# Kernel tuning notes

Hardware: AMD Instinct MI355X
Metric: run time of the kernel (lower is better)

## Reference

```python
import jax, jax.numpy as jnp
import numpy as np

H = 8
BLEN = 256
NEG = -1e9

def _mask2d(blen, h=32, win=6):
    # precomputed 2D-local mask for tail blocks: query pos in [blen, 2blen),
    # key pos in [0, 2blen); causal + Chebyshev-ish window on a width-h image grid
    cp = np.arange(blen, 2 * blen)[:, None]
    op = np.arange(2 * blen)[None, :]
    causal = op <= cp
    ch, cw = cp // h, cp % h
    oh, ow = op // h, op % h
    ok = causal & (np.abs(ch - oh) <= win) & (np.abs(cw - ow) <= win)
    return np.where(ok, 0.0, NEG).astype(np.float32)

def _causal_mask(blen):
    return np.where(np.tril(np.ones((blen, blen), bool)), 0.0, NEG).astype(np.float32)

def _attn(X, Wq, Wk, Wv, Wo):
    B, L, D = X.shape
    dh = D // H
    split = lambda Y: Y.reshape(B, L, H, dh).transpose(0, 2, 1, 3)  # [B,H,L,dh]
    q = split(X @ Wq) * (dh ** -0.5)
    k = split(X @ Wk)
    v = split(X @ Wv)
    pad = (-L) % BLEN
    if pad:
        q, k, v = (jnp.pad(t, ((0, 0), (0, 0), (0, pad), (0, 0))) for t in (q, k, v))
    Lp = L + pad
    n = Lp // BLEN
    bias1 = jnp.asarray(_causal_mask(BLEN))
    logits1 = jnp.einsum('bhqd,bhkd->bhqk', q[:, :, :BLEN], k[:, :, :BLEN]) + bias1
    first = jax.nn.softmax(logits1, axis=-1) @ v[:, :, :BLEN]  # [B,H,BLEN,dh]
    if n > 1:
        qb = q.reshape(B, H, n, BLEN, dh)
        kb = k.reshape(B, H, n, BLEN, dh)
        vb = v.reshape(B, H, n, BLEN, dh)
        local_k = jnp.concatenate([kb[:, :, :-1], kb[:, :, 1:]], axis=3)  # [B,H,n-1,2B,dh]
        local_v = jnp.concatenate([vb[:, :, :-1], vb[:, :, 1:]], axis=3)
        bias2 = jnp.asarray(_mask2d(BLEN))
        logits2 = jnp.einsum('bhnqd,bhnkd->bhnqk', qb[:, :, 1:], local_k) + bias2
        tail = jnp.einsum('bhnqk,bhnkd->bhnqd', jax.nn.softmax(logits2, axis=-1), local_v)
        tail = tail.reshape(B, H, (n - 1) * BLEN, dh)
        res = jnp.concatenate([first, tail], axis=2)[:, :, :L]
    else:
        res = first[:, :, :L]
    res = res.transpose(0, 2, 1, 3).reshape(B, L, D)
    return res @ Wo

def _ln(x, g, b, eps=1e-6):
    m = x.mean(-1, keepdims=True)
    v = ((x - m) ** 2).mean(-1, keepdims=True)
    return (x - m) / jnp.sqrt(v + eps) * g + b

def setup_inputs() -> dict:
    key = jax.random.key(0)
    ks = jax.random.split(key, 8)
    D, F = 256, 512
    s = 0.02
    return {
        'X': jax.random.normal(ks[0], (32, 1024, D), jnp.float32),
        'Wq': jax.random.normal(ks[1], (D, D), jnp.float32) * s,
        'Wk': jax.random.normal(ks[2], (D, D), jnp.float32) * s,
        'Wv': jax.random.normal(ks[3], (D, D), jnp.float32) * s,
        'Wo': jax.random.normal(ks[4], (D, D), jnp.float32) * s,
        'ln1_g': jnp.ones((D,), jnp.float32),
        'ln1_b': jnp.zeros((D,), jnp.float32),
        'W1': jax.random.normal(ks[5], (D, F), jnp.float32) * s,
        'b1': jnp.zeros((F,), jnp.float32),
        'W2': jax.random.normal(ks[6], (F, D), jnp.float32) * s,
        'b2': jnp.zeros((D,), jnp.float32),
        'ln2_g': jnp.ones((D,), jnp.float32),
        'ln2_b': jnp.zeros((D,), jnp.float32),
    }

def reference(X, Wq, Wk, Wv, Wo, ln1_g, ln1_b, W1, b1, W2, b2, ln2_g, ln2_b):
    y = _attn(X, Wq, Wk, Wv, Wo)
    X = _ln(y + X, ln1_g, ln1_b)
    y = jax.nn.relu(X @ W1 + b1) @ W2 + b2
    return _ln(y + X, ln2_g, ln2_b)
```

## Files before the change

kernel.cpp:

```cpp
#include <hip/hip_runtime.h>

typedef unsigned short u16;
typedef __attribute__((ext_vector_type(8))) short bh8;
typedef __attribute__((ext_vector_type(4))) short s4;
typedef __attribute__((ext_vector_type(4))) short bh4;
typedef __attribute__((ext_vector_type(4))) float fx4;

__device__ __forceinline__ u16 f2b(float f) {
  union { float f; unsigned u; } v; v.f = f;
  unsigned r = v.u + 0x7fffu + ((v.u >> 16) & 1u);
  return (u16)(r >> 16);
}
__device__ __forceinline__ float b2f(u16 h) {
  union { unsigned u; float f; } v; v.u = ((unsigned)h) << 16; return v.f;
}

__device__ __forceinline__ float ex2(float x) {
#if __has_builtin(__builtin_amdgcn_exp2f)
  return __builtin_amdgcn_exp2f(x);
#else
  return __expf(x * 0.6931471805599453f);
#endif
}

__device__ __forceinline__ unsigned cvtpk(float lo, float hi) {
  unsigned r;
  asm("v_cvt_pk_bf16_f32 %0, %1, %2" : "=v"(r) : "v"(lo), "v"(hi));
  return r;
}

#if __has_builtin(__builtin_amdgcn_mfma_f32_16x16x16bf16_1k)
__device__ __forceinline__ fx4 pv_mfma(s4 a, s4 b, fx4 c) {
  return __builtin_amdgcn_mfma_f32_16x16x16bf16_1k(a, b, c, 0, 0, 0);
}
#else
__device__ __forceinline__ fx4 pv_mfma(s4 a, s4 b, fx4 c) {
  asm("v_mfma_f32_16x16x16_bf16 %0, %1, %2, %0" : "+v"(c) : "v"(a), "v"(b));
  return c;
}
#endif

__global__ __launch_bounds__(256) void conv_x_k(const float* __restrict__ X, u16* __restrict__ Xb) {
  int i = blockIdx.x * 256 + threadIdx.x;
  float4 v = ((const float4*)X)[i];
  bh4 o; o[0]=(short)f2b(v.x); o[1]=(short)f2b(v.y); o[2]=(short)f2b(v.z); o[3]=(short)f2b(v.w);
  ((bh4*)Xb)[i] = o;
}

__global__ __launch_bounds__(256) void conv_w_k(const float* __restrict__ Wq, const float* __restrict__ Wk,
                         const float* __restrict__ Wv, const float* __restrict__ Wo,
                         const float* __restrict__ W1, const float* __restrict__ W2,
                         u16* __restrict__ WqkvT, u16* __restrict__ WoT,
                         u16* __restrict__ W1T, u16* __restrict__ W2T) {
  int i = blockIdx.x * 256 + threadIdx.x;
  if (i < 196608) {
    int n = i >> 8, k = i & 255; float v;
    if (n < 256) v = Wq[k*256+n] * 0.25503487359f;
    else if (n < 512) v = Wk[k*256+(n-256)];
    else v = Wv[k*256+(n-512)];
    WqkvT[i] = f2b(v);
  } else if (i < 262144) {
    int j = i - 196608; int n = j >> 8, k = j & 255;
    WoT[j] = f2b(Wo[k*256+n]);
  } else if (i < 393216) {
    int j = i - 262144; int n = j >> 8, k = j & 255;
    W1T[j] = f2b(W1[k*512+n]);
  } else {
    int j = i - 393216; int n = j >> 9, k = j & 511;
    W2T[j] = f2b(W2[k*256+n]);
  }
}

template<int K, int N, int EPI>
__global__ __launch_bounds__(256) void gemm_k(
    const u16* __restrict__ A, const u16* __restrict__ BT,
    u16* __restrict__ C0, u16* __restrict__ C1, u16* __restrict__ C2,
    const float* __restrict__ bias) {
  constexpr int BK = 32;
  __shared__ u16 smem[16384];
  const int nx = gridDim.x;
  const int lid = blockIdx.y * nx + blockIdx.x;
  const int xcd = lid & 7;
  const int jj2 = lid >> 3;
  const int m0 = (xcd * (gridDim.y >> 3) + jj2 / nx) * 128;
  const int n0 = (jj2 % nx) * 128;
  const int tid = threadIdx.x, lane = tid & 63, wv = tid >> 6;
  const int wr = wv >> 1, wc = wv & 1, lg = lane >> 4, ll = lane & 15;

  fx4 acc[4][4] = {};

  auto stage = [&](int buf, int ks) {
#pragma unroll
    for (int i = 0; i < 2; ++i) {
      int c = i*256 + tid;
      int row = c >> 2, ko = (c & 3) * 8;
      const u16* gpA = A  + (size_t)(m0+row)*K + ks + ko;
      const u16* gpB = BT + (size_t)(n0+row)*K + ks + ko;
      int lbase = (i*256 + wv*64) * 8;
      __builtin_amdgcn_global_load_lds((const __attribute__((address_space(1))) void*)gpA,
          (__attribute__((address_space(3))) void*)&smem[buf*4096 + lbase], 16, 0, 0);
      __builtin_amdgcn_global_load_lds((const __attribute__((address_space(1))) void*)gpB,
          (__attribute__((address_space(3))) void*)&smem[8192 + buf*4096 + lbase], 16, 0, 0);
    }
  };

  constexpr int NT = K / BK;
  stage(0, 0);
  __syncthreads();
  int cur = 0;
  for (int t = 0; t < NT; ++t) {
    if (t + 1 < NT) stage(cur ^ 1, (t+1)*BK);
    bh8 af[4], bfr[4];
#pragma unroll
    for (int mi = 0; mi < 4; ++mi)
      af[mi] = *(const bh8*)&smem[cur*4096 + (wr*64 + mi*16 + ll)*BK + lg*8];
#pragma unroll
    for (int ni = 0; ni < 4; ++ni)
      bfr[ni] = *(const bh8*)&smem[8192 + cur*4096 + (wc*64 + ni*16 + ll)*BK + lg*8];
#pragma unroll
    for (int mi = 0; mi < 4; ++mi)
#pragma unroll
      for (int ni = 0; ni < 4; ++ni)
        acc[mi][ni] = __builtin_amdgcn_mfma_f32_16x16x32_bf16(af[mi], bfr[ni], acc[mi][ni], 0, 0, 0);
    __syncthreads();
    cur ^= 1;
  }

  auto swz = [](int r) { return ((r & 14) << 2) ^ ((r & 3) << 5); };
  const bool vt = (EPI == 0) && (n0 >= 512);

  if (!vt) {
    float bv[4];
    if constexpr (EPI >= 2) {
#pragma unroll
      for (int ni = 0; ni < 4; ++ni) bv[ni] = bias[n0 + wc*64 + ni*16 + ll];
    }
#pragma unroll
    for (int mi = 0; mi < 4; ++mi)
#pragma unroll
      for (int ni = 0; ni < 4; ++ni) {
        fx4 v = acc[mi][ni];
        int n = wc*64 + ni*16 + ll;
#pragma unroll
        for (int ii = 0; ii < 2; ++ii) {
          float x0 = v[2*ii], x1 = v[2*ii+1];
          if constexpr (EPI == 2) { x0 = fmaxf(x0 + bv[ni], 0.f); x1 = fmaxf(x1 + bv[ni], 0.f); }
          else if constexpr (EPI == 3) { x0 += bv[ni]; x1 += bv[ni]; }
          unsigned pk = cvtpk(x0, x1);
          int mA = wr*64 + mi*16 + lg*4 + 2*ii;
          int mB = mA + 1;
          smem[mA*128 + (n ^ swz(mA))] = (u16)pk;
          smem[mB*128 + (n ^ swz(mB))] = (u16)(pk >> 16);
        }
      }
  } else {
#pragma unroll
    for (int mi = 0; mi < 4; ++mi)
#pragma unroll
      for (int ni = 0; ni < 4; ++ni) {
        fx4 v = acc[mi][ni];
        int n = wc*64 + ni*16 + ll;
        int mb = wr*64 + mi*16 + lg*4;
        uint2 pk;
        pk.x = cvtpk(v[0], v[1]);
        pk.y = cvtpk(v[2], v[3]);
        *(uint2*)&smem[n*128 + (mb ^ swz(n))] = pk;
      }
  }
  __syncthreads();

#pragma unroll
  for (int j = 0; j < 8; ++j) {
    int cid = tid + 256*j;
    int row = cid >> 4, c8 = (cid & 15) << 3;
    bh8 val = *(const bh8*)&smem[row*128 + (c8 ^ swz(row))];
    if constexpr (EPI == 0) {
      if (!vt) {
        int m = m0 + row; int b = m >> 10, l = m & 1023;
        int n = n0 + c8; int hh = (n >> 5) & 7, d = n & 31;
        size_t bh_ = (size_t)(b*8 + hh);
        u16* dst = (n0 < 256) ? C0 : C1;
        *(bh8*)&dst[(bh_*1024 + l)*32 + d] = val;
      } else {
        int n = n0 + row; int hh = (n >> 5) & 7, d = n & 31;
        int m = m0 + c8; int b = m >> 10, l = m & 1023;
        size_t bh_ = (size_t)(b*8 + hh);
        *(bh8*)&C2[(bh_*32 + d)*1024 + l] = val;
      }
    } else {
      *(bh8*)&C0[(size_t)(m0+row)*N + n0 + c8] = val;
    }
  }
}

__global__ __launch_bounds__(256) void attn_k(
    const u16* __restrict__ qw, const u16* __restrict__ kw,
    const u16* __restrict__ vtw, u16* __restrict__ ao) {
  const int qb = blockIdx.x, hh = blockIdx.y, b = blockIdx.z;
  const int tid = threadIdx.x, lane = tid & 63, wv = tid >> 6;
  const int lg = lane >> 4, ll = lane & 15;
  const int kstart = qb ? (qb - 1) * 256 : 0;
  const size_t bh_ = (size_t)(b*8 + hh);
  const u16* kg = kw  + (bh_*1024 + kstart)*32;
  const u16* vg = vtw + bh_*32*1024 + kstart;
  const u16* qg = qw  + (bh_*1024 + qb*256)*32;

  bh8 qf[4];
#pragma unroll
  for (int qi = 0; qi < 4; ++qi)
    qf[qi] = *(const bh8*)&qg[(size_t)(wv*64 + qi*16 + ll)*32 + lg*8];

  fx4 oacc[4][2] = {};
  float lsum[4] = {0.f, 0.f, 0.f, 0.f};
  const fx4 zero = {0.f, 0.f, 0.f, 0.f};

  const int ch0 = wv*2;
  const int lo_w = qb ? ch0 + 2 : 0;
  const int hi_w = qb ? ch0 + 9 : ch0 + 1;

  for (int ohm = lo_w; ohm <= hi_w; ++ohm) {
    const int kb = ohm * 32;
    bh8 kf0 = *(const bh8*)&kg[(size_t)(kb + ll)*32 + lg*8];
    bh8 kf1 = *(const bh8*)&kg[(size_t)(kb + 16 + ll)*32 + lg*8];
    s4 vb[2][2];
#pragma unroll
    for (int cs = 0; cs < 2; ++cs)
#pragma unroll
      for (int dsub = 0; dsub < 2; ++dsub)
        vb[cs][dsub] = *(const s4*)&vg[(size_t)(dsub*16 + ll)*1024 + kb + cs*16 + lg*4];

#pragma unroll
    for (int qi = 0; qi < 4; ++qi) {
      const int ch = ch0 + (qi >> 1);
      const int dlo = qb ? ch + 2 : 0;
      const int dhi = qb ? ch + 8 : ch;
      if (ohm < dlo || ohm > dhi) continue;
      const bool diag = (ohm == dhi);

      fx4 s0 = __builtin_amdgcn_mfma_f32_16x16x32_bf16(kf0, qf[qi], zero, 0, 0, 0);
      fx4 s1 = __builtin_amdgcn_mfma_f32_16x16x32_bf16(kf1, qf[qi], zero, 0, 0, 0);

      const int cw = ll + ((qi & 1) << 4);
      float p[2][4];
      if (!qb && !diag) {
#pragma unroll
        for (int i = 0; i < 4; ++i) { p[0][i] = ex2(s0[i]); p[1][i] = ex2(s1[i]); }
      } else {
        const int off = (qb && !diag) ? 6 : 0;
        const unsigned thr = diag ? (qb ? 7u : 32u) : 13u;
#pragma unroll
        for (int cs = 0; cs < 2; ++cs) {
          const int tb = cw + off - cs*16 - lg*4;
          fx4 sv = cs ? s1 : s0;
#pragma unroll
          for (int i = 0; i < 4; ++i) {
            bool ok = (unsigned)(tb - i) < thr;
            p[cs][i] = ok ? ex2(sv[i]) : 0.f;
          }
        }
      }
      lsum[qi] += (p[0][0]+p[0][1]+p[0][2]+p[0][3]) + (p[1][0]+p[1][1]+p[1][2]+p[1][3]);

#pragma unroll
      for (int cs = 0; cs < 2; ++cs) {
        union { unsigned u[2]; s4 s; } cv;
        cv.u[0] = cvtpk(p[cs][0], p[cs][1]);
        cv.u[1] = cvtpk(p[cs][2], p[cs][3]);
#pragma unroll
        for (int dsub = 0; dsub < 2; ++dsub)
          oacc[qi][dsub] = pv_mfma(cv.s, vb[cs][dsub], oacc[qi][dsub]);
      }
    }
  }

  float rinv[4];
#pragma unroll
  for (int qi = 0; qi < 4; ++qi) {
    float v = lsum[qi];
    v += __shfl_xor(v, 16);
    v += __shfl_xor(v, 32);
    rinv[qi] = 1.0f / v;
  }

  u16* aop = ao + ((size_t)(b*1024 + qb*256))*256 + hh*32;
#pragma unroll
  for (int qi = 0; qi < 4; ++qi) {
    float rq[4];
#pragma unroll
    for (int i = 0; i < 4; ++i) rq[i] = __shfl(rinv[qi], lg*4 + i);
#pragma unroll
    for (int dsub = 0; dsub < 2; ++dsub)
#pragma unroll
      for (int i = 0; i < 4; ++i) {
        int q = wv*64 + qi*16 + lg*4 + i;
        aop[(size_t)q*256 + dsub*16 + ll] = f2b(oacc[qi][dsub][i] * rq[i]);
      }
  }
}

template<int XF32, int OF32>
__global__ __launch_bounds__(256) void ln_k(
    const u16* __restrict__ y, const void* __restrict__ xres,
    const float* __restrict__ g, const float* __restrict__ bb,
    void* __restrict__ out) {
  int row = blockIdx.x*4 + (threadIdx.x >> 6);
  int lane = threadIdx.x & 63;
  int c0 = lane * 4;
  size_t base = (size_t)row * 256 + c0;
  bh4 yv = *(const bh4*)&y[base];
  float s[4];
  if constexpr (XF32) {
    float4 xv = *(const float4*)&((const float*)xres)[base];
    s[0] = b2f((u16)yv[0]) + xv.x; s[1] = b2f((u16)yv[1]) + xv.y;
    s[2] = b2f((u16)yv[2]) + xv.z; s[3] = b2f((u16)yv[3]) + xv.w;
  } else {
    bh4 xv = *(const bh4*)&((const u16*)xres)[base];
#pragma unroll
    for (int j = 0; j < 4; ++j) s[j] = b2f((u16)yv[j]) + b2f((u16)xv[j]);
  }
  float sum = s[0]+s[1]+s[2]+s[3];
  float sq  = s[0]*s[0]+s[1]*s[1]+s[2]*s[2]+s[3]*s[3];
#pragma unroll
  for (int m = 1; m <= 32; m <<= 1) { sum += __shfl_xor(sum, m); sq += __shfl_xor(sq, m); }
  float mean = sum * 0.00390625f;
  float var  = sq  * 0.00390625f - mean*mean;
  float rs = rsqrtf(var + 1e-6f);
  float4 gv = *(const float4*)&g[c0];
  float4 bv = *(const float4*)&bb[c0];
  if constexpr (OF32) {
    float4 o;
    o.x = (s[0]-mean)*rs*gv.x + bv.x; o.y = (s[1]-mean)*rs*gv.y + bv.y;
    o.z = (s[2]-mean)*rs*gv.z + bv.z; o.w = (s[3]-mean)*rs*gv.w + bv.w;
    *(float4*)&((float*)out)[base] = o;
  } else {
    bh4 o;
    o[0] = (short)f2b((s[0]-mean)*rs*gv.x + bv.x);
    o[1] = (short)f2b((s[1]-mean)*rs*gv.y + bv.y);
    o[2] = (short)f2b((s[2]-mean)*rs*gv.z + bv.z);
    o[3] = (short)f2b((s[3]-mean)*rs*gv.w + bv.w);
    *(bh4*)&((u16*)out)[base] = o;
  }
}

extern "C" void kernel_launch(void* const* d_in, const int* in_sizes, int n_in,
                              void* d_out, int out_size, void* d_ws, size_t ws_size,
                              hipStream_t stream) {
  const float* X    = (const float*)d_in[0];
  const float* Wq   = (const float*)d_in[1];
  const float* Wk   = (const float*)d_in[2];
  const float* Wv   = (const float*)d_in[3];
  const float* Wo   = (const float*)d_in[4];
  const float* ln1g = (const float*)d_in[5];
  const float* ln1b = (const float*)d_in[6];
  const float* W1   = (const float*)d_in[7];
  const float* b1   = (const float*)d_in[8];
  const float* W2   = (const float*)d_in[9];
  const float* b2   = (const float*)d_in[10];
  const float* ln2g = (const float*)d_in[11];
  const float* ln2b = (const float*)d_in[12];
  float* out = (float*)d_out;

  char* ws = (char*)d_ws;
  const size_t A = 32768ull * 256 * 2;
  u16* Xb  = (u16*)(ws);
  u16* qws = (u16*)(ws + A);
  u16* kws = (u16*)(ws + 2*A);
  u16* vtw = (u16*)(ws + 3*A);
  u16* ao  = Xb;
  u16* yw  = qws;
  u16* x1b = kws;
  u16* y2  = vtw;
  u16* hw  = Xb;
  u16* WqkvT = (u16*)(ws + 4*A);
  u16* WoT = WqkvT + 196608;
  u16* W1T = WoT + 65536;
  u16* W2T = W1T + 131072;

  conv_x_k<<<8192, 256, 0, stream>>>(X, Xb);
  conv_w_k<<<2048, 256, 0, stream>>>(Wq, Wk, Wv, Wo, W1, W2, WqkvT, WoT, W1T, W2T);
  gemm_k<256, 768, 0><<<dim3(6, 256), 256, 0, stream>>>(Xb, WqkvT, qws, kws, vtw, nullptr);
  attn_k<<<dim3(4, 8, 32), 256, 0, stream>>>(qws, kws, vtw, ao);
  gemm_k<256, 256, 1><<<dim3(2, 256), 256, 0, stream>>>(ao, WoT, yw, nullptr, nullptr, nullptr);
  ln_k<1, 0><<<8192, 256, 0, stream>>>(yw, X, ln1g, ln1b, x1b);
  gemm_k<256, 512, 2><<<dim3(4, 256), 256, 0, stream>>>(x1b, W1T, hw, nullptr, nullptr, b1);
  gemm_k<512, 256, 3><<<dim3(2, 256), 256, 0, stream>>>(hw, W2T, y2, nullptr, nullptr, b2);
  ln_k<0, 1><<<8192, 256, 0, stream>>>(y2, x1b, ln2g, ln2b, out);
}
```

Baseline: 133.8 us.

## Fuse X bf16 conversion into QKV GEMM and LayerNorms into output GEMMs

Removes the separate X fp32-to-bf16 conversion kernel by having the QKV GEMM load fp32 A tiles into registers, convert them and write them to LDS. Adds a new GEMM+LayerNorm kernel that computes full 256-wide output rows per 64-row block, then applies the residual add, bias and LayerNorm in the epilogue. This replaces the Wo GEMM plus LN1 and the W2 GEMM plus LN2 pairs, cutting launches and round trips of intermediates through global memory. The trade-off is register-staged fp32 loads in the QKV GEMM and a narrower M tile with a full-N tile in the fused kernels, which may lower per-block parallelism.

```diff
diff --git a/kernel.cpp b/kernel.cpp
--- a/kernel.cpp
+++ b/kernel.cpp
@@ -39,13 +39,6 @@
   return c;
 }
 #endif
-
-__global__ __launch_bounds__(256) void conv_x_k(const float* __restrict__ X, u16* __restrict__ Xb) {
-  int i = blockIdx.x * 256 + threadIdx.x;
-  float4 v = ((const float4*)X)[i];
-  bh4 o; o[0]=(short)f2b(v.x); o[1]=(short)f2b(v.y); o[2]=(short)f2b(v.z); o[3]=(short)f2b(v.w);
-  ((bh4*)Xb)[i] = o;
-}
 
 __global__ __launch_bounds__(256) void conv_w_k(const float* __restrict__ Wq, const float* __restrict__ Wk,
                          const float* __restrict__ Wv, const float* __restrict__ Wo,
@@ -71,9 +64,9 @@
   }
 }
 
-template<int K, int N, int EPI>
+template<int K, int N, int EPI, int AF32>
 __global__ __launch_bounds__(256) void gemm_k(
-    const u16* __restrict__ A, const u16* __restrict__ BT,
+    const void* __restrict__ Av, const u16* __restrict__ BT,
     u16* __restrict__ C0, u16* __restrict__ C1, u16* __restrict__ C2,
     const float* __restrict__ bias) {
   constexpr int BK = 32;
@@ -86,30 +79,64 @@
   const int n0 = (jj2 % nx) * 128;
   const int tid = threadIdx.x, lane = tid & 63, wv = tid >> 6;
   const int wr = wv >> 1, wc = wv & 1, lg = lane >> 4, ll = lane & 15;
+  const u16* A16 = (const u16*)Av;
+  const float* A32 = (const float*)Av;
 
   fx4 acc[4][4] = {};
 
-  auto stage = [&](int buf, int ks) {
+  auto stageB = [&](int buf, int ks) {
 #pragma unroll
     for (int i = 0; i < 2; ++i) {
       int c = i*256 + tid;
       int row = c >> 2, ko = (c & 3) * 8;
-      const u16* gpA = A  + (size_t)(m0+row)*K + ks + ko;
       const u16* gpB = BT + (size_t)(n0+row)*K + ks + ko;
+      int lbase = (i*256 + wv*64) * 8;
+      __builtin_amdgcn_global_load_lds((const __attribute__((address_space(1))) void*)gpB,
+          (__attribute__((address_space(3))) void*)&smem[8192 + buf*4096 + lbase], 16, 0, 0);
+    }
+  };
+  auto stageA16 = [&](int buf, int ks) {
+#pragma unroll
+    for (int i = 0; i < 2; ++i) {
+      int c = i*256 + tid;
+      int row = c >> 2, ko = (c & 3) * 8;
+      const u16* gpA = A16 + (size_t)(m0+row)*K + ks + ko;
       int lbase = (i*256 + wv*64) * 8;
       __builtin_amdgcn_global_load_lds((const __attribute__((address_space(1))) void*)gpA,
           (__attribute__((address_space(3))) void*)&smem[buf*4096 + lbase], 16, 0, 0);
-      __builtin_amdgcn_global_load_lds((const __attribute__((address_space(1))) void*)gpB,
-          (__attribute__((address_space(3))) void*)&smem[8192 + buf*4096 + lbase], 16, 0, 0);
     }
   };
+  float4 apf[4];
+  auto loadA32 = [&](int ks) {
+#pragma unroll
+    for (int i = 0; i < 4; ++i) {
+      int c = i*256 + tid;
+      int row = c >> 3, c4 = (c & 7) * 4;
+      apf[i] = *(const float4*)&A32[(size_t)(m0+row)*K + ks + c4];
+    }
+  };
+  auto writeA32 = [&](int buf) {
+#pragma unroll
+    for (int i = 0; i < 4; ++i) {
+      int c = i*256 + tid;
+      int row = c >> 3, c4 = (c & 7) * 4;
+      uint2 pk;
+      pk.x = cvtpk(apf[i].x, apf[i].y);
+      pk.y = cvtpk(apf[i].z, apf[i].w);
+      *(uint2*)&smem[buf*4096 + row*32 + c4] = pk;
+    }
+  };
 
   constexpr int NT = K / BK;
-  stage(0, 0);
+  if constexpr (AF32) { loadA32(0); writeA32(0); } else stageA16(0, 0);
+  stageB(0, 0);
   __syncthreads();
   int cur = 0;
   for (int t = 0; t < NT; ++t) {
-    if (t + 1 < NT) stage(cur ^ 1, (t+1)*BK);
+    if (t + 1 < NT) {
+      if constexpr (AF32) loadA32((t+1)*BK); else stageA16(cur ^ 1, (t+1)*BK);
+      stageB(cur ^ 1, (t+1)*BK);
+    }
     bh8 af[4], bfr[4];
 #pragma unroll
     for (int mi = 0; mi < 4; ++mi)
@@ -122,6 +149,7 @@
 #pragma unroll
       for (int ni = 0; ni < 4; ++ni)
         acc[mi][ni] = __builtin_amdgcn_mfma_f32_16x16x32_bf16(af[mi], bfr[ni], acc[mi][ni], 0, 0, 0);
+    if constexpr (AF32) { if (t + 1 < NT) writeA32(cur ^ 1); }
     __syncthreads();
     cur ^= 1;
   }
@@ -145,7 +173,6 @@
         for (int ii = 0; ii < 2; ++ii) {
           float x0 = v[2*ii], x1 = v[2*ii+1];
           if constexpr (EPI == 2) { x0 = fmaxf(x0 + bv[ni], 0.f); x1 = fmaxf(x1 + bv[ni], 0.f); }
-          else if constexpr (EPI == 3) { x0 += bv[ni]; x1 += bv[ni]; }
           unsigned pk = cvtpk(x0, x1);
           int mA = wr*64 + mi*16 + lg*4 + 2*ii;
           int mB = mA + 1;
@@ -193,6 +220,131 @@
   }
 }
 
+template<int K, int RF32, int OF32, int BIAS>
+__global__ __launch_bounds__(256) void gemm_ln_k(
+    const u16* __restrict__ A, const u16* __restrict__ BT,
+    const void* __restrict__ resid, const float* __restrict__ bias,
+    const float* __restrict__ g, const float* __restrict__ b,
+    void* __restrict__ out) {
+  constexpr int BK = 32;
+  __shared__ u16 smem[20480];
+  const int lid = blockIdx.y;
+  const int xcd = lid & 7;
+  const int jj2 = lid >> 3;
+  const int m0 = (xcd * (gridDim.y >> 3) + jj2) * 64;
+  const int tid = threadIdx.x, lane = tid & 63, wv = tid >> 6;
+  const int wr = wv >> 1, wc = wv & 1, lg = lane >> 4, ll = lane & 15;
+
+  fx4 acc[2][8] = {};
+
+  auto stage = [&](int buf, int ks) {
+    {
+      int c = tid;
+      int row = c >> 2, ko = (c & 3) * 8;
+      const u16* gpA = A + (size_t)(m0+row)*K + ks + ko;
+      int lbase = wv*512;
+      __builtin_amdgcn_global_load_lds((const __attribute__((address_space(1))) void*)gpA,
+          (__attribute__((address_space(3))) void*)&smem[buf*2048 + lbase], 16, 0, 0);
+    }
+#pragma unroll
+    for (int i = 0; i < 4; ++i) {
+      int c = i*256 + tid;
+      int row = c >> 2, ko = (c & 3) * 8;
+      const u16* gpB = BT + (size_t)row*K + ks + ko;
+      int lbase = (i*256 + wv*64) * 8;
+      __builtin_amdgcn_global_load_lds((const __attribute__((address_space(1))) void*)gpB,
+          (__attribute__((address_space(3))) void*)&smem[4096 + buf*8192 + lbase], 16, 0, 0);
+    }
+  };
+
+  constexpr int NT = K / BK;
+  stage(0, 0);
+  __syncthreads();
+  int cur = 0;
+  for (int t = 0; t < NT; ++t) {
+    if (t + 1 < NT) stage(cur ^ 1, (t+1)*BK);
+    bh8 af[2], bfr[8];
+#pragma unroll
+    for (int mi = 0; mi < 2; ++mi)
+      af[mi] = *(const bh8*)&smem[cur*2048 + (wr*32 + mi*16 + ll)*BK + lg*8];
+#pragma unroll
+    for (int ni = 0; ni < 8; ++ni)
+      bfr[ni] = *(const bh8*)&smem[4096 + cur*8192 + (wc*128 + ni*16 + ll)*BK + lg*8];
+#pragma unroll
+    for (int mi = 0; mi < 2; ++mi)
+#pragma unroll
+      for (int ni = 0; ni < 8; ++ni)
+        acc[mi][ni] = __builtin_amdgcn_mfma_f32_16x16x32_bf16(bfr[ni], af[mi], acc[mi][ni], 0, 0, 0);
+    __syncthreads();
+    cur ^= 1;
+  }
+
+#pragma unroll
+  for (int mi = 0; mi < 2; ++mi) {
+    int m_l = wr*32 + mi*16 + ll;
+    int sx = (m_l & 7) << 1;
+#pragma unroll
+    for (int ni = 0; ni < 8; ++ni) {
+      fx4 v = acc[mi][ni];
+      int gidx = (wc*32 + ni*4 + lg) ^ sx;
+      uint2 pk;
+      pk.x = cvtpk(v[0], v[1]);
+      pk.y = cvtpk(v[2], v[3]);
+      *(uint2*)&smem[m_l*256 + gidx*4] = pk;
+    }
+  }
+  __syncthreads();
+
+  const int c0 = lane * 4;
+  float4 gv = *(const float4*)&g[c0];
+  float4 bv = *(const float4*)&b[c0];
+  float4 biasv = {0.f, 0.f, 0.f, 0.f};
+  if constexpr (BIAS) biasv = *(const float4*)&bias[c0];
+#pragma unroll 4
+  for (int rr = 0; rr < 16; ++rr) {
+    int r = wv*16 + rr;
+    bh4 yv = *(const bh4*)&smem[r*256 + ((lane ^ ((r & 7) << 1)) << 2)];
+    size_t gbase = (size_t)(m0 + r) * 256 + c0;
+    float s0, s1, s2, s3;
+    if constexpr (RF32) {
+      float4 xv = *(const float4*)&((const float*)resid)[gbase];
+      s0 = b2f((u16)yv[0]) + biasv.x + xv.x;
+      s1 = b2f((u16)yv[1]) + biasv.y + xv.y;
+      s2 = b2f((u16)yv[2]) + biasv.z + xv.z;
+      s3 = b2f((u16)yv[3]) + biasv.w + xv.w;
+    } else {
+      bh4 xv = *(const bh4*)&((const u16*)resid)[gbase];
+      s0 = b2f((u16)yv[0]) + biasv.x + b2f((u16)xv[0]);
+      s1 = b2f((u16)yv[1]) + biasv.y + b2f((u16)xv[1]);
+      s2 = b2f((u16)yv[2]) + biasv.z + b2f((u16)xv[2]);
+      s3 = b2f((u16)yv[3]) + biasv.w + b2f((u16)xv[3]);
+    }
+    float sum = s0 + s1 + s2 + s3;
+    float sq  = s0*s0 + s1*s1 + s2*s2 + s3*s3;
+#pragma unroll
+    for (int msk = 1; msk <= 32; msk <<= 1) {
+      sum += __shfl_xor(sum, msk);
+      sq  += __shfl_xor(sq, msk);
+    }
+    float mean = sum * 0.00390625f;
+    float var  = sq  * 0.00390625f - mean*mean;
+    float rs = rsqrtf(var + 1e-6f);
+    float o0 = (s0 - mean)*rs*gv.x + bv.x;
+    float o1 = (s1 - mean)*rs*gv.y + bv.y;
+    float o2 = (s2 - mean)*rs*gv.z + bv.z;
+    float o3 = (s3 - mean)*rs*gv.w + bv.w;
+    if constexpr (OF32) {
+      float4 o = {o0, o1, o2, o3};
+      *(float4*)&((float*)out)[gbase] = o;
+    } else {
+      bh4 o;
+      o[0] = (short)f2b(o0); o[1] = (short)f2b(o1);
+      o[2] = (short)f2b(o2); o[3] = (short)f2b(o3);
+      *(bh4*)&((u16*)out)[gbase] = o;
+    }
+  }
+}
+
 __global__ __launch_bounds__(256) void attn_k(
     const u16* __restrict__ qw, const u16* __restrict__ kw,
     const u16* __restrict__ vtw, u16* __restrict__ ao) {
@@ -295,50 +447,6 @@
         int q = wv*64 + qi*16 + lg*4 + i;
         aop[(size_t)q*256 + dsub*16 + ll] = f2b(oacc[qi][dsub][i] * rq[i]);
       }
-  }
-}
-
-template<int XF32, int OF32>
-__global__ __launch_bounds__(256) void ln_k(
-    const u16* __restrict__ y, const void* __restrict__ xres,
-    const float* __restrict__ g, const float* __restrict__ bb,
-    void* __restrict__ out) {
-  int row = blockIdx.x*4 + (threadIdx.x >> 6);
-  int lane = threadIdx.x & 63;
-  int c0 = lane * 4;
-  size_t base = (size_t)row * 256 + c0;
-  bh4 yv = *(const bh4*)&y[base];
-  float s[4];
-  if constexpr (XF32) {
-    float4 xv = *(const float4*)&((const float*)xres)[base];
-    s[0] = b2f((u16)yv[0]) + xv.x; s[1] = b2f((u16)yv[1]) + xv.y;
-    s[2] = b2f((u16)yv[2]) + xv.z; s[3] = b2f((u16)yv[3]) + xv.w;
-  } else {
-    bh4 xv = *(const bh4*)&((const u16*)xres)[base];
-#pragma unroll
-    for (int j = 0; j < 4; ++j) s[j] = b2f((u16)yv[j]) + b2f((u16)xv[j]);
-  }
-  float sum = s[0]+s[1]+s[2]+s[3];
-  float sq  = s[0]*s[0]+s[1]*s[1]+s[2]*s[2]+s[3]*s[3];
-#pragma unroll
-  for (int m = 1; m <= 32; m <<= 1) { sum += __shfl_xor(sum, m); sq += __shfl_xor(sq, m); }
-  float mean = sum * 0.00390625f;
-  float var  = sq  * 0.00390625f - mean*mean;
-  float rs = rsqrtf(var + 1e-6f);
-  float4 gv = *(const float4*)&g[c0];
-  float4 bv = *(const float4*)&bb[c0];
-  if constexpr (OF32) {
-    float4 o;
-    o.x = (s[0]-mean)*rs*gv.x + bv.x; o.y = (s[1]-mean)*rs*gv.y + bv.y;
-    o.z = (s[2]-mean)*rs*gv.z + bv.z; o.w = (s[3]-mean)*rs*gv.w + bv.w;
-    *(float4*)&((float*)out)[base] = o;
-  } else {
-    bh4 o;
-    o[0] = (short)f2b((s[0]-mean)*rs*gv.x + bv.x);
-    o[1] = (short)f2b((s[1]-mean)*rs*gv.y + bv.y);
-    o[2] = (short)f2b((s[2]-mean)*rs*gv.z + bv.z);
-    o[3] = (short)f2b((s[3]-mean)*rs*gv.w + bv.w);
-    *(bh4*)&((u16*)out)[base] = o;
   }
 }
 
@@ -362,27 +470,21 @@
 
   char* ws = (char*)d_ws;
   const size_t A = 32768ull * 256 * 2;
-  u16* Xb  = (u16*)(ws);
   u16* qws = (u16*)(ws + A);
   u16* kws = (u16*)(ws + 2*A);
   u16* vtw = (u16*)(ws + 3*A);
-  u16* ao  = Xb;
-  u16* yw  = qws;
+  u16* ao  = (u16*)(ws);
   u16* x1b = kws;
-  u16* y2  = vtw;
-  u16* hw  = Xb;
+  u16* hw  = (u16*)(ws);
   u16* WqkvT = (u16*)(ws + 4*A);
   u16* WoT = WqkvT + 196608;
   u16* W1T = WoT + 65536;
   u16* W2T = W1T + 131072;
 
-  conv_x_k<<<8192, 256, 0, stream>>>(X, Xb);
   conv_w_k<<<2048, 256, 0, stream>>>(Wq, Wk, Wv, Wo, W1, W2, WqkvT, WoT, W1T, W2T);
-  gemm_k<256, 768, 0><<<dim3(6, 256), 256, 0, stream>>>(Xb, WqkvT, qws, kws, vtw, nullptr);
+  gemm_k<256, 768, 0, 1><<<dim3(6, 256), 256, 0, stream>>>(X, WqkvT, qws, kws, vtw, nullptr);
   attn_k<<<dim3(4, 8, 32), 256, 0, stream>>>(qws, kws, vtw, ao);
-  gemm_k<256, 256, 1><<<dim3(2, 256), 256, 0, stream>>>(ao, WoT, yw, nullptr, nullptr, nullptr);
-  ln_k<1, 0><<<8192, 256, 0, stream>>>(yw, X, ln1g, ln1b, x1b);
-  gemm_k<256, 512, 2><<<dim3(4, 256), 256, 0, stream>>>(x1b, W1T, hw, nullptr, nullptr, b1);
-  gemm_k<512, 256, 3><<<dim3(2, 256), 256, 0, stream>>>(hw, W2T, y2, nullptr, nullptr, b2);
-  ln_k<0, 1><<<8192, 256, 0, stream>>>(y2, x1b, ln2g, ln2b, out);
-}
+  gemm_ln_k<256, 1, 0, 0><<<dim3(1, 512), 256, 0, stream>>>(ao, WoT, X, nullptr, ln1g, ln1b, x1b);
+  gemm_k<256, 512, 2, 0><<<dim3(4, 256), 256, 0, stream>>>(x1b, W1T, hw, nullptr, nullptr, b1);
+  gemm_ln_k<512, 0, 1, 1><<<dim3(1, 512), 256, 0, stream>>>(hw, W2T, x1b, b2, ln2g, ln2b, out);
+}
```

New measurement: 120.1 us. 10.2% less time.
